# Optimization experiments

Measured on AMD Instinct MI355X. Metric: run time of the kernel, lower is better.

The kernel has to match this reference:

```python
import jax, jax.numpy as jnp
import numpy as np

B, L, D = 4, 4096, 1024
K_LEN = 128  # decay kernel taps


def setup_inputs() -> dict:
    key = jax.random.key(0)
    k1, k2, k3 = jax.random.split(key, 3)
    x = jax.random.normal(k1, (B, L, D), dtype=jnp.float32)
    W_qkv = jax.random.normal(k2, (3 * D, D), dtype=jnp.float32) * 0.02
    W_out = jax.random.normal(k3, (D, D), dtype=jnp.float32) * 0.02
    # matches torch init: exp(-linspace(0, 10, 128))
    decay_kernel = jnp.exp(-jnp.linspace(0.0, 10.0, K_LEN)).astype(jnp.float32)
    return {"x": x, "W_qkv": W_qkv, "W_out": W_out, "decay_kernel": decay_kernel}


def reference(x, W_qkv, W_out, decay_kernel):
    # qkv projection (bias=False): [B,L,D] @ [D,3D] -> split into q,k,v
    qkv = jnp.einsum('bld,ed->ble', x, W_qkv)
    q, k, v = jnp.split(qkv, 3, axis=-1)
    src = k * v  # [B,L,D]
    K = decay_kernel.shape[0]
    N = x.shape[1] + K - 1  # full linear-conv length
    src_f = jnp.fft.rfft(src, n=N, axis=1)                 # [B,N//2+1,D] complex
    kern_f = jnp.fft.rfft(decay_kernel, n=N)[None, :, None]  # same kernel per channel
    res = jnp.fft.irfft(src_f * kern_f, n=N, axis=1)[:, :x.shape[1], :]  # causal slice
    out = q * res  # q-gating
    # dropout is identity in eval mode
    return jnp.einsum('bld,ed->ble', out, W_out)
```

## Files before the change

### kernel.cpp

```cpp
#include <hip/hip_runtime.h>

#define BDIM 4
#define LDIM 4096
#define DDIM 1024
#define KTAPS 128
#define LCHUNK 64

typedef __attribute__((ext_vector_type(8))) _Float16 f16x8;
typedef __attribute__((ext_vector_type(16))) float f32x16;

__device__ __forceinline__ float f16_to_f(ushort h) {
    return (float)__builtin_bit_cast(_Float16, h);
}
__device__ __forceinline__ ushort f_to_f16(float f) {
    return __builtin_bit_cast(ushort, (_Float16)f);
}

__device__ __forceinline__ void load_lds16(const ushort* g, ushort* l) {
    __builtin_amdgcn_global_load_lds(
        (const __attribute__((address_space(1))) void*)g,
        (__attribute__((address_space(3))) void*)l, 16, 0, 0);
}

#define NSWZ(r) ((((r) & 3) ^ (((r) >> 2) & 3)))

#define NX4 (BDIM * LDIM * DDIM / 4)
#define NQ4 (3 * DDIM * DDIM / 4)
#define NO4 (DDIM * DDIM / 4)
__global__ __launch_bounds__(256) void to_f16_all(const float* __restrict__ x,
                                                  const float* __restrict__ wq,
                                                  const float* __restrict__ wo,
                                                  ushort* __restrict__ xh,
                                                  ushort* __restrict__ wqh,
                                                  ushort* __restrict__ woh) {
    const int ntot = NX4 + NQ4 + NO4;
    for (int i = blockIdx.x * 256 + threadIdx.x; i < ntot; i += gridDim.x * 256) {
        const float* src;
        ushort* dst;
        int j = i;
        if (j < NX4) {
            src = x; dst = xh;
        } else if (j < NX4 + NQ4) {
            j -= NX4; src = wq; dst = wqh;
        } else {
            j -= NX4 + NQ4; src = wo; dst = woh;
        }
        const float4 v = *(const float4*)&src[(size_t)j * 4];
        ushort4 h;
        h.x = f_to_f16(v.x);
        h.y = f_to_f16(v.y);
        h.z = f_to_f16(v.z);
        h.w = f_to_f16(v.w);
        *(ushort4*)&dst[(size_t)j * 4] = h;
    }
}

template <int OBF>
__global__ __launch_bounds__(256) void gemm_f16(const ushort* __restrict__ A,
                                                const ushort* __restrict__ B,
                                                void* __restrict__ Cp, int ldc, int Kc) {
    __shared__ ushort As[128 * 32];
    __shared__ ushort Bs[128 * 32];

    const int tid = threadIdx.x;

    const int gx = gridDim.x;
    const int nwg = gx * gridDim.y;
    const int orig = blockIdx.y * gx + blockIdx.x;
    const int q8 = nwg >> 3;
    const int tile = (orig & 7) * q8 + (orig >> 3);
    const int m0 = (tile / gx) * 128;
    const int n0 = (tile % gx) * 128;

    const int ra = tid >> 2;
    const int ga = tid & 3;
    const int gs = (ga ^ NSWZ(ra)) * 8;

    const ushort* srcA0 = A + (size_t)(m0 + ra) * Kc + gs;
    const ushort* srcA1 = A + (size_t)(m0 + 64 + ra) * Kc + gs;
    const ushort* srcB0 = B + (size_t)(n0 + ra) * Kc + gs;
    const ushort* srcB1 = B + (size_t)(n0 + 64 + ra) * Kc + gs;
    ushort* dstA0 = &As[tid * 8];
    ushort* dstA1 = &As[(tid + 256) * 8];
    ushort* dstB0 = &Bs[tid * 8];
    ushort* dstB1 = &Bs[(tid + 256) * 8];

    const int lane = tid & 63;
    const int w = tid >> 6;
    const int wr = w >> 1, wc = w & 1;
    const int l31 = lane & 31;
    const int hi = lane >> 5;
    const int nsw = NSWZ(l31 & 15);
    const int arow = wr * 64 + l31;
    const int brow = wc * 64 + l31;

    f32x16 acc[2][2] = {};

    for (int kc = 0; kc < Kc; kc += 32) {
        __syncthreads();
        load_lds16(srcA0, dstA0);
        load_lds16(srcA1, dstA1);
        load_lds16(srcB0, dstB0);
        load_lds16(srcB1, dstB1);
        srcA0 += 32; srcA1 += 32; srcB0 += 32; srcB1 += 32;
        __syncthreads();

        f16x8 a[2][2], b[2][2];
#pragma unroll
        for (int rb = 0; rb < 2; ++rb)
#pragma unroll
            for (int kh = 0; kh < 2; ++kh)
                a[rb][kh] = *(const f16x8*)&As[(arow + rb * 32) * 32 +
                                               (((2 * kh + hi) ^ nsw) * 8)];
#pragma unroll
        for (int cb = 0; cb < 2; ++cb)
#pragma unroll
            for (int kh = 0; kh < 2; ++kh)
                b[cb][kh] = *(const f16x8*)&Bs[(brow + cb * 32) * 32 +
                                               (((2 * kh + hi) ^ nsw) * 8)];
#pragma unroll
        for (int rb = 0; rb < 2; ++rb)
#pragma unroll
            for (int cb = 0; cb < 2; ++cb) {
                acc[rb][cb] = __builtin_amdgcn_mfma_f32_32x32x16_f16(
                    a[rb][0], b[cb][0], acc[rb][cb], 0, 0, 0);
                acc[rb][cb] = __builtin_amdgcn_mfma_f32_32x32x16_f16(
                    a[rb][1], b[cb][1], acc[rb][cb], 0, 0, 0);
            }
    }

#pragma unroll
    for (int rb = 0; rb < 2; ++rb)
#pragma unroll
        for (int cb = 0; cb < 2; ++cb) {
            const int colb = n0 + wc * 64 + cb * 32 + l31;
            const int rowb = m0 + wr * 64 + rb * 32 + 4 * hi;
#pragma unroll
            for (int q = 0; q < 16; ++q) {
                const int row = rowb + (q & 3) + 8 * (q >> 2);
                if (OBF) {
                    ((ushort*)Cp)[(size_t)row * ldc + colb] = f_to_f16(acc[rb][cb][q]);
                } else {
                    ((float*)Cp)[(size_t)row * ldc + colb] = acc[rb][cb][q];
                }
            }
        }
}

__global__ __launch_bounds__(256) void conv_gate_f16(const ushort* __restrict__ qkvh,
                                                     const float* __restrict__ decay,
                                                     ushort* __restrict__ gh) {
    __shared__ float sdec[KTAPS];
    if (threadIdx.x < KTAPS) sdec[threadIdx.x] = decay[threadIdx.x];
    __syncthreads();

    const int d = blockIdx.y * 256 + threadIdx.x;
    const int b = blockIdx.z;
    const int l0 = blockIdx.x * LCHUNK;

    const float r = sdec[1];
    const float dlast = r * sdec[KTAPS - 1];
    const size_t rs = 3 * DDIM;

    const ushort* base = qkvh + (size_t)b * LDIM * rs;
    const ushort* qc = base + d;
    const ushort* kc = base + DDIM + d;
    const ushort* vc = base + 2 * DDIM + d;
    ushort* g0 = gh + (size_t)b * LDIM * DDIM + d;

    float res = 0.f;
    int lstart;
    if (l0 == 0) {
        lstart = 0;
    } else {
        const int tmax = (l0 < KTAPS - 1) ? l0 : (KTAPS - 1);
#pragma unroll 4
        for (int t = 0; t <= tmax; ++t) {
            const size_t off = (size_t)(l0 - t) * rs;
            res += sdec[t] * f16_to_f(kc[off]) * f16_to_f(vc[off]);
        }
        g0[(size_t)l0 * DDIM] = f_to_f16(f16_to_f(qc[(size_t)l0 * rs]) * res);
        lstart = l0 + 1;
    }

    for (int l = lstart; l < l0 + LCHUNK; ++l) {
        const size_t off = (size_t)l * rs;
        const float s = f16_to_f(kc[off]) * f16_to_f(vc[off]);
        if (l == 0) {
            res = sdec[0] * s;
        } else {
            float sub = 0.f;
            if (l >= KTAPS) {
                const size_t o2 = (size_t)(l - KTAPS) * rs;
                sub = dlast * f16_to_f(kc[o2]) * f16_to_f(vc[o2]);
            }
            res = r * res + s - sub;
        }
        g0[(size_t)l * DDIM] = f_to_f16(f16_to_f(qc[off]) * res);
    }
}

extern "C" void kernel_launch(void* const* d_in, const int* in_sizes, int n_in,
                              void* d_out, int out_size, void* d_ws, size_t ws_size,
                              hipStream_t stream) {
    const float* x = (const float*)d_in[0];
    const float* Wqkv = (const float*)d_in[1];
    const float* Wout = (const float*)d_in[2];
    const float* decay = (const float*)d_in[3];

    const int M = BDIM * LDIM;
    const size_t MB = 1024 * 1024;

    ushort* qkvh = (ushort*)d_ws;
    ushort* gh = (ushort*)((char*)d_ws + 96 * MB);
    ushort* xh = (ushort*)((char*)d_ws + 128 * MB);
    ushort* wqkvh = (ushort*)((char*)d_ws + 160 * MB);
    ushort* wouth = (ushort*)((char*)d_ws + 166 * MB);

    to_f16_all<<<2048, 256, 0, stream>>>(x, Wqkv, Wout, xh, wqkvh, wouth);

    dim3 g1(3 * DDIM / 128, M / 128);
    gemm_f16<1><<<g1, 256, 0, stream>>>(xh, wqkvh, qkvh, 3 * DDIM, DDIM);

    dim3 g2(LDIM / LCHUNK, DDIM / 256, BDIM);
    conv_gate_f16<<<g2, 256, 0, stream>>>(qkvh, decay, gh);

    dim3 g3(DDIM / 128, M / 128);
    gemm_f16<0><<<g3, 256, 0, stream>>>(gh, wouth, d_out, DDIM, DDIM);
}
```

Before: 283.4 us.

## Double-buffer GEMM LDS tiles and enlarge conv chunk length

The GEMM now keeps two LDS buffers and issues the global-to-LDS loads for the next K tile before computing on the current one, with a single barrier per iteration. The aim is to hide global load latency behind the MFMA work, at the cost of doubling LDS per block, which may reduce occupancy. The conv chunk length is also doubled, which halves the recompute of the warm-up window per chunk but also halves the number of blocks. The single barrier relies on the hardware waiting for outstanding LDS-DMA loads before it, which may not be guaranteed without an explicit vmcnt wait.

```diff
diff --git a/kernel.cpp b/kernel.cpp
--- a/kernel.cpp
+++ b/kernel.cpp
@@ -4,7 +4,7 @@
 #define LDIM 4096
 #define DDIM 1024
 #define KTAPS 128
-#define LCHUNK 64
+#define LCHUNK 128
 
 typedef __attribute__((ext_vector_type(8))) _Float16 f16x8;
 typedef __attribute__((ext_vector_type(16))) float f32x16;
@@ -59,8 +59,8 @@
 __global__ __launch_bounds__(256) void gemm_f16(const ushort* __restrict__ A,
                                                 const ushort* __restrict__ B,
                                                 void* __restrict__ Cp, int ldc, int Kc) {
-    __shared__ ushort As[128 * 32];
-    __shared__ ushort Bs[128 * 32];
+    __shared__ ushort As[2][128 * 32];
+    __shared__ ushort Bs[2][128 * 32];
 
     const int tid = threadIdx.x;
 
@@ -80,10 +80,6 @@
     const ushort* srcA1 = A + (size_t)(m0 + 64 + ra) * Kc + gs;
     const ushort* srcB0 = B + (size_t)(n0 + ra) * Kc + gs;
     const ushort* srcB1 = B + (size_t)(n0 + 64 + ra) * Kc + gs;
-    ushort* dstA0 = &As[tid * 8];
-    ushort* dstA1 = &As[(tid + 256) * 8];
-    ushort* dstB0 = &Bs[tid * 8];
-    ushort* dstB1 = &Bs[(tid + 256) * 8];
 
     const int lane = tid & 63;
     const int w = tid >> 6;
@@ -93,31 +89,38 @@
     const int nsw = NSWZ(l31 & 15);
     const int arow = wr * 64 + l31;
     const int brow = wc * 64 + l31;
+    const int NT = Kc >> 5;
 
     f32x16 acc[2][2] = {};
 
-    for (int kc = 0; kc < Kc; kc += 32) {
-        __syncthreads();
-        load_lds16(srcA0, dstA0);
-        load_lds16(srcA1, dstA1);
-        load_lds16(srcB0, dstB0);
-        load_lds16(srcB1, dstB1);
-        srcA0 += 32; srcA1 += 32; srcB0 += 32; srcB1 += 32;
-        __syncthreads();
+    auto STAGE = [&](const int buf, const int kt) {
+        const int ko = kt * 32;
+        load_lds16(srcA0 + ko, &As[buf][tid * 8]);
+        load_lds16(srcA1 + ko, &As[buf][(tid + 256) * 8]);
+        load_lds16(srcB0 + ko, &Bs[buf][tid * 8]);
+        load_lds16(srcB1 + ko, &Bs[buf][(tid + 256) * 8]);
+    };
+
+    STAGE(0, 0);
+    __syncthreads();
+
+    for (int t = 0; t < NT; ++t) {
+        const int cur = t & 1;
+        if (t + 1 < NT) STAGE(cur ^ 1, t + 1);
 
         f16x8 a[2][2], b[2][2];
 #pragma unroll
         for (int rb = 0; rb < 2; ++rb)
 #pragma unroll
             for (int kh = 0; kh < 2; ++kh)
-                a[rb][kh] = *(const f16x8*)&As[(arow + rb * 32) * 32 +
-                                               (((2 * kh + hi) ^ nsw) * 8)];
+                a[rb][kh] = *(const f16x8*)&As[cur][(arow + rb * 32) * 32 +
+                                                   (((2 * kh + hi) ^ nsw) * 8)];
 #pragma unroll
         for (int cb = 0; cb < 2; ++cb)
 #pragma unroll
             for (int kh = 0; kh < 2; ++kh)
-                b[cb][kh] = *(const f16x8*)&Bs[(brow + cb * 32) * 32 +
-                                               (((2 * kh + hi) ^ nsw) * 8)];
+                b[cb][kh] = *(const f16x8*)&Bs[cur][(brow + cb * 32) * 32 +
+                                                   (((2 * kh + hi) ^ nsw) * 8)];
 #pragma unroll
         for (int rb = 0; rb < 2; ++rb)
 #pragma unroll
@@ -127,6 +130,8 @@
                 acc[rb][cb] = __builtin_amdgcn_mfma_f32_32x32x16_f16(
                     a[rb][1], b[cb][1], acc[rb][cb], 0, 0, 0);
             }
+
+        __syncthreads();
     }
 
 #pragma unroll
```

Result: slower. 332.9 us (+17.4%).

## Fuse x fp32-to-f16 conversion into QKV GEMM and pack conv channel pairs

Applied to the files above, without the earlier changes.

Drops the separate conversion pass over x. The QKV GEMM now reads fp32 x directly, converts it to f16 in registers, writes it to LDS, and prefetches the next tile ahead of the barrier. The conv/gate kernel now handles two channels per thread with 32-bit packed loads and stores, using 128 threads per block. This saves a full write and reread of the f16 copy of x. In exchange the GEMM reads twice as many bytes for A through non-LDS-direct loads, and the conv kernel has half as many threads in flight.

```diff
diff --git a/kernel.cpp b/kernel.cpp
--- a/kernel.cpp
+++ b/kernel.cpp
@@ -24,41 +24,22 @@
 
 #define NSWZ(r) ((((r) & 3) ^ (((r) >> 2) & 3)))
 
-#define NX4 (BDIM * LDIM * DDIM / 4)
-#define NQ4 (3 * DDIM * DDIM / 4)
-#define NO4 (DDIM * DDIM / 4)
-__global__ __launch_bounds__(256) void to_f16_all(const float* __restrict__ x,
-                                                  const float* __restrict__ wq,
-                                                  const float* __restrict__ wo,
-                                                  ushort* __restrict__ xh,
-                                                  ushort* __restrict__ wqh,
-                                                  ushort* __restrict__ woh) {
-    const int ntot = NX4 + NQ4 + NO4;
-    for (int i = blockIdx.x * 256 + threadIdx.x; i < ntot; i += gridDim.x * 256) {
-        const float* src;
-        ushort* dst;
-        int j = i;
-        if (j < NX4) {
-            src = x; dst = xh;
-        } else if (j < NX4 + NQ4) {
-            j -= NX4; src = wq; dst = wqh;
-        } else {
-            j -= NX4 + NQ4; src = wo; dst = woh;
-        }
-        const float4 v = *(const float4*)&src[(size_t)j * 4];
+__global__ __launch_bounds__(256) void to_f16(const float* __restrict__ in,
+                                              ushort* __restrict__ out, int n4) {
+    for (int i = blockIdx.x * 256 + threadIdx.x; i < n4; i += gridDim.x * 256) {
+        const float4 v = *(const float4*)&in[(size_t)i * 4];
         ushort4 h;
         h.x = f_to_f16(v.x);
         h.y = f_to_f16(v.y);
         h.z = f_to_f16(v.z);
         h.w = f_to_f16(v.w);
-        *(ushort4*)&dst[(size_t)j * 4] = h;
-    }
-}
-
-template <int OBF>
-__global__ __launch_bounds__(256) void gemm_f16(const ushort* __restrict__ A,
+        *(ushort4*)&out[(size_t)i * 4] = h;
+    }
+}
+
+__global__ __launch_bounds__(256) void gemm1_xa(const float* __restrict__ X,
                                                 const ushort* __restrict__ B,
-                                                void* __restrict__ Cp, int ldc, int Kc) {
+                                                ushort* __restrict__ C, int ldc, int Kc) {
     __shared__ ushort As[128 * 32];
     __shared__ ushort Bs[128 * 32];
 
@@ -76,14 +57,10 @@
     const int ga = tid & 3;
     const int gs = (ga ^ NSWZ(ra)) * 8;
 
-    const ushort* srcA0 = A + (size_t)(m0 + ra) * Kc + gs;
-    const ushort* srcA1 = A + (size_t)(m0 + 64 + ra) * Kc + gs;
+    const float* xs0 = X + (size_t)(m0 + ra) * Kc + gs;
+    const float* xs1 = X + (size_t)(m0 + 64 + ra) * Kc + gs;
     const ushort* srcB0 = B + (size_t)(n0 + ra) * Kc + gs;
     const ushort* srcB1 = B + (size_t)(n0 + 64 + ra) * Kc + gs;
-    ushort* dstA0 = &As[tid * 8];
-    ushort* dstA1 = &As[(tid + 256) * 8];
-    ushort* dstB0 = &Bs[tid * 8];
-    ushort* dstB1 = &Bs[(tid + 256) * 8];
 
     const int lane = tid & 63;
     const int w = tid >> 6;
@@ -93,15 +70,125 @@
     const int nsw = NSWZ(l31 & 15);
     const int arow = wr * 64 + l31;
     const int brow = wc * 64 + l31;
+    const int NT = Kc >> 5;
+
+    f32x16 acc[2][2] = {};
+    float4 a0lo, a0hi, a1lo, a1hi;
+
+    auto ALOAD = [&](const int kt) {
+        const float* p0 = xs0 + kt * 32;
+        const float* p1 = xs1 + kt * 32;
+        a0lo = *(const float4*)p0;
+        a0hi = *(const float4*)(p0 + 4);
+        a1lo = *(const float4*)p1;
+        a1hi = *(const float4*)(p1 + 4);
+    };
+    auto PACK = [](const float4 u, const float4 v) {
+        f16x8 r;
+        r[0] = (_Float16)u.x; r[1] = (_Float16)u.y;
+        r[2] = (_Float16)u.z; r[3] = (_Float16)u.w;
+        r[4] = (_Float16)v.x; r[5] = (_Float16)v.y;
+        r[6] = (_Float16)v.z; r[7] = (_Float16)v.w;
+        return r;
+    };
+
+    ALOAD(0);
+    for (int t = 0; t < NT; ++t) {
+        __syncthreads();
+        load_lds16(srcB0 + t * 32, &Bs[tid * 8]);
+        load_lds16(srcB1 + t * 32, &Bs[(tid + 256) * 8]);
+        *(f16x8*)&As[tid * 8] = PACK(a0lo, a0hi);
+        *(f16x8*)&As[(tid + 256) * 8] = PACK(a1lo, a1hi);
+        if (t + 1 < NT) {
+            ALOAD(t + 1);
+            asm volatile("s_waitcnt vmcnt(4) lgkmcnt(0)" ::: "memory");
+        } else {
+            asm volatile("s_waitcnt vmcnt(0) lgkmcnt(0)" ::: "memory");
+        }
+        __builtin_amdgcn_sched_barrier(0);
+        __builtin_amdgcn_s_barrier();
+
+        f16x8 a[2][2], b[2][2];
+#pragma unroll
+        for (int rb = 0; rb < 2; ++rb)
+#pragma unroll
+            for (int kh = 0; kh < 2; ++kh)
+                a[rb][kh] = *(const f16x8*)&As[(arow + rb * 32) * 32 +
+                                              (((2 * kh + hi) ^ nsw) * 8)];
+#pragma unroll
+        for (int cb = 0; cb < 2; ++cb)
+#pragma unroll
+            for (int kh = 0; kh < 2; ++kh)
+                b[cb][kh] = *(const f16x8*)&Bs[(brow + cb * 32) * 32 +
+                                              (((2 * kh + hi) ^ nsw) * 8)];
+#pragma unroll
+        for (int rb = 0; rb < 2; ++rb)
+#pragma unroll
+            for (int cb = 0; cb < 2; ++cb) {
+                acc[rb][cb] = __builtin_amdgcn_mfma_f32_32x32x16_f16(
+                    a[rb][0], b[cb][0], acc[rb][cb], 0, 0, 0);
+                acc[rb][cb] = __builtin_amdgcn_mfma_f32_32x32x16_f16(
+                    a[rb][1], b[cb][1], acc[rb][cb], 0, 0, 0);
+            }
+    }
+
+#pragma unroll
+    for (int rb = 0; rb < 2; ++rb)
+#pragma unroll
+        for (int cb = 0; cb < 2; ++cb) {
+            const int colb = n0 + wc * 64 + cb * 32 + l31;
+            const int rowb = m0 + wr * 64 + rb * 32 + 4 * hi;
+#pragma unroll
+            for (int q = 0; q < 16; ++q) {
+                const int row = rowb + (q & 3) + 8 * (q >> 2);
+                C[(size_t)row * ldc + colb] = f_to_f16(acc[rb][cb][q]);
+            }
+        }
+}
+
+template <int OBF>
+__global__ __launch_bounds__(256) void gemm_f16(const ushort* __restrict__ A,
+                                                const ushort* __restrict__ B,
+                                                void* __restrict__ Cp, int ldc, int Kc) {
+    __shared__ ushort As[128 * 32];
+    __shared__ ushort Bs[128 * 32];
+
+    const int tid = threadIdx.x;
+
+    const int gx = gridDim.x;
+    const int nwg = gx * gridDim.y;
+    const int orig = blockIdx.y * gx + blockIdx.x;
+    const int q8 = nwg >> 3;
+    const int tile = (orig & 7) * q8 + (orig >> 3);
+    const int m0 = (tile / gx) * 128;
+    const int n0 = (tile % gx) * 128;
+
+    const int ra = tid >> 2;
+    const int ga = tid & 3;
+    const int gs = (ga ^ NSWZ(ra)) * 8;
+
+    const ushort* srcA0 = A + (size_t)(m0 + ra) * Kc + gs;
+    const ushort* srcA1 = A + (size_t)(m0 + 64 + ra) * Kc + gs;
+    const ushort* srcB0 = B + (size_t)(n0 + ra) * Kc + gs;
+    const ushort* srcB1 = B + (size_t)(n0 + 64 + ra) * Kc + gs;
+
+    const int lane = tid & 63;
+    const int w = tid >> 6;
+    const int wr = w >> 1, wc = w & 1;
+    const int l31 = lane & 31;
+    const int hi = lane >> 5;
+    const int nsw = NSWZ(l31 & 15);
+    const int arow = wr * 64 + l31;
+    const int brow = wc * 64 + l31;
 
     f32x16 acc[2][2] = {};
 
     for (int kc = 0; kc < Kc; kc += 32) {
         __syncthreads();
-        load_lds16(srcA0, dstA0);
-        load_lds16(srcA1, dstA1);
-        load_lds16(srcB0, dstB0);
-        load_lds16(srcB1, dstB1);
+        load_lds16(srcA0, &As[tid * 8]);
+        load_lds16(srcA1, &As[(tid + 256) * 8]);
+        load_lds16(srcB0, &Bs[tid * 8]);
+        load_lds16(srcB1, &Bs[(tid + 256) * 8]);
         srcA0 += 32; srcA1 += 32; srcB0 += 32; srcB1 += 32;
         __syncthreads();
 
@@ -111,13 +198,13 @@
 #pragma unroll
             for (int kh = 0; kh < 2; ++kh)
                 a[rb][kh] = *(const f16x8*)&As[(arow + rb * 32) * 32 +
-                                               (((2 * kh + hi) ^ nsw) * 8)];
+                                              (((2 * kh + hi) ^ nsw) * 8)];
 #pragma unroll
         for (int cb = 0; cb < 2; ++cb)
 #pragma unroll
             for (int kh = 0; kh < 2; ++kh)
                 b[cb][kh] = *(const f16x8*)&Bs[(brow + cb * 32) * 32 +
-                                               (((2 * kh + hi) ^ nsw) * 8)];
+                                              (((2 * kh + hi) ^ nsw) * 8)];
 #pragma unroll
         for (int rb = 0; rb < 2; ++rb)
 #pragma unroll
@@ -147,28 +234,33 @@
         }
 }
 
-__global__ __launch_bounds__(256) void conv_gate_f16(const ushort* __restrict__ qkvh,
+__device__ __forceinline__ float2 up2(uint u) {
+    return make_float2(f16_to_f((ushort)(u & 0xffff)), f16_to_f((ushort)(u >> 16)));
+}
+
+__global__ __launch_bounds__(128) void conv_gate_f16(const ushort* __restrict__ qkvh,
                                                      const float* __restrict__ decay,
                                                      ushort* __restrict__ gh) {
     __shared__ float sdec[KTAPS];
-    if (threadIdx.x < KTAPS) sdec[threadIdx.x] = decay[threadIdx.x];
+    sdec[threadIdx.x] = decay[threadIdx.x];
     __syncthreads();
 
-    const int d = blockIdx.y * 256 + threadIdx.x;
+    const int dp = blockIdx.y * 128 + threadIdx.x;
     const int b = blockIdx.z;
     const int l0 = blockIdx.x * LCHUNK;
 
     const float r = sdec[1];
     const float dlast = r * sdec[KTAPS - 1];
-    const size_t rs = 3 * DDIM;
-
-    const ushort* base = qkvh + (size_t)b * LDIM * rs;
-    const ushort* qc = base + d;
-    const ushort* kc = base + DDIM + d;
-    const ushort* vc = base + 2 * DDIM + d;
-    ushort* g0 = gh + (size_t)b * LDIM * DDIM + d;
-
-    float res = 0.f;
+    const int rsu = 3 * DDIM / 2;
+    const int gsu = DDIM / 2;
+
+    const uint* basep = (const uint*)(qkvh + (size_t)b * LDIM * 3 * DDIM);
+    const uint* qc = basep + dp;
+    const uint* kc = basep + DDIM / 2 + dp;
+    const uint* vc = basep + DDIM + dp;
+    uint* g0 = (uint*)(gh + (size_t)b * LDIM * DDIM) + dp;
+
+    float res0 = 0.f, res1 = 0.f;
     int lstart;
     if (l0 == 0) {
         lstart = 0;
@@ -176,27 +268,38 @@
         const int tmax = (l0 < KTAPS - 1) ? l0 : (KTAPS - 1);
 #pragma unroll 4
         for (int t = 0; t <= tmax; ++t) {
-            const size_t off = (size_t)(l0 - t) * rs;
-            res += sdec[t] * f16_to_f(kc[off]) * f16_to_f(vc[off]);
-        }
-        g0[(size_t)l0 * DDIM] = f_to_f16(f16_to_f(qc[(size_t)l0 * rs]) * res);
+            const size_t off = (size_t)(l0 - t) * rsu;
+            const float2 kk = up2(kc[off]), vv = up2(vc[off]);
+            res0 += sdec[t] * kk.x * vv.x;
+            res1 += sdec[t] * kk.y * vv.y;
+        }
+        const float2 qq = up2(qc[(size_t)l0 * rsu]);
+        g0[(size_t)l0 * gsu] = (uint)f_to_f16(qq.x * res0) |
+                               ((uint)f_to_f16(qq.y * res1) << 16);
         lstart = l0 + 1;
     }
 
     for (int l = lstart; l < l0 + LCHUNK; ++l) {
-        const size_t off = (size_t)l * rs;
-        const float s = f16_to_f(kc[off]) * f16_to_f(vc[off]);
+        const size_t off = (size_t)l * rsu;
+        const float2 kk = up2(kc[off]), vv = up2(vc[off]);
+        const float s0 = kk.x * vv.x, s1 = kk.y * vv.y;
         if (l == 0) {
-            res = sdec[0] * s;
+            res0 = sdec[0] * s0;
+            res1 = sdec[0] * s1;
         } else {
-            float sub = 0.f;
+            float sub0 = 0.f, sub1 = 0.f;
             if (l >= KTAPS) {
-                const size_t o2 = (size_t)(l - KTAPS) * rs;
-                sub = dlast * f16_to_f(kc[o2]) * f16_to_f(vc[o2]);
-            }
-            res = r * res + s - sub;
-        }
-        g0[(size_t)l * DDIM] = f_to_f16(f16_to_f(qc[off]) * res);
+                const size_t o2 = (size_t)(l - KTAPS) * rsu;
+                const float2 k2 = up2(kc[o2]), v2 = up2(vc[o2]);
+                sub0 = dlast * k2.x * v2.x;
+                sub1 = dlast * k2.y * v2.y;
+            }
+            res0 = r * res0 + s0 - sub0;
+            res1 = r * res1 + s1 - sub1;
+        }
+        const float2 qq = up2(qc[off]);
+        g0[(size_t)l * gsu] = (uint)f_to_f16(qq.x * res0) |
+                              ((uint)f_to_f16(qq.y * res1) << 16);
     }
 }
 
@@ -213,17 +316,17 @@
 
     ushort* qkvh = (ushort*)d_ws;
     ushort* gh = (ushort*)((char*)d_ws + 96 * MB);
-    ushort* xh = (ushort*)((char*)d_ws + 128 * MB);
-    ushort* wqkvh = (ushort*)((char*)d_ws + 160 * MB);
-    ushort* wouth = (ushort*)((char*)d_ws + 166 * MB);
-
-    to_f16_all<<<2048, 256, 0, stream>>>(x, Wqkv, Wout, xh, wqkvh, wouth);
+    ushort* wqkvh = (ushort*)((char*)d_ws + 128 * MB);
+    ushort* wouth = (ushort*)((char*)d_ws + 134 * MB);
+
+    to_f16<<<512, 256, 0, stream>>>(Wqkv, wqkvh, 3 * DDIM * DDIM / 4);
+    to_f16<<<256, 256, 0, stream>>>(Wout, wouth, DDIM * DDIM / 4);
 
     dim3 g1(3 * DDIM / 128, M / 128);
-    gemm_f16<1><<<g1, 256, 0, stream>>>(xh, wqkvh, qkvh, 3 * DDIM, DDIM);
+    gemm1_xa<<<g1, 256, 0, stream>>>(x, wqkvh, qkvh, 3 * DDIM, DDIM);
 
     dim3 g2(LDIM / LCHUNK, DDIM / 256, BDIM);
-    conv_gate_f16<<<g2, 256, 0, stream>>>(qkvh, decay, gh);
+    conv_gate_f16<<<g2, 128, 0, stream>>>(qkvh, decay, gh);
 
     dim3 g3(DDIM / 128, M / 128);
     gemm_f16<0><<<g3, 256, 0, stream>>>(gh, wouth, d_out, DDIM, DDIM);
```

New measurement: 330.9 us. 16.7% more time.
